# Kernel tuning notes

Measured on AMD Instinct MI355X. Metric: run time of the kernel, lower is better.

Reference implementation:

```python
import jax, jax.numpy as jnp
import numpy as np

VOCAB, DIM, HEADS, LAYERS = 32000, 1024, 16, 2
B, S = 2, 1024
HD = DIM // HEADS


def rmsnorm(x, g, eps=1e-6):
    return x * jax.lax.rsqrt(jnp.mean(x * x, axis=-1, keepdims=True) + eps) * g


def setup_inputs() -> dict:
    key = jax.random.key(0)
    ks = jax.random.split(key, 20)
    s = 0.02
    d = {
        "text_ids": jax.random.randint(ks[0], (B, S), 0, VOCAB),
        "embed": jax.random.normal(ks[1], (VOCAB, DIM), jnp.float32) * s,
        "g1": jnp.ones((LAYERS, DIM), jnp.float32),
        "wq": jax.random.normal(ks[2], (LAYERS, DIM, DIM), jnp.float32) * s,
        "bq": jnp.zeros((LAYERS, DIM), jnp.float32),
        "wk": jax.random.normal(ks[3], (LAYERS, DIM, DIM), jnp.float32) * s,
        "bk": jnp.zeros((LAYERS, DIM), jnp.float32),
        "wv": jax.random.normal(ks[4], (LAYERS, DIM, DIM), jnp.float32) * s,
        "bv": jnp.zeros((LAYERS, DIM), jnp.float32),
        "wo": jax.random.normal(ks[5], (LAYERS, DIM, DIM), jnp.float32) * s,
        "bo": jnp.zeros((LAYERS, DIM), jnp.float32),
        "g2": jnp.ones((LAYERS, DIM), jnp.float32),
        "w1": jax.random.normal(ks[6], (LAYERS, DIM, 4 * DIM), jnp.float32) * s,
        "b1": jnp.zeros((LAYERS, 4 * DIM), jnp.float32),
        "w2": jax.random.normal(ks[7], (LAYERS, 4 * DIM, DIM), jnp.float32) * s,
        "b2": jnp.zeros((LAYERS, DIM), jnp.float32),
        "gf": jnp.ones((DIM,), jnp.float32),
        "head_w": jax.random.normal(ks[8], (DIM, VOCAB), jnp.float32) * s,
        "head_b": jnp.zeros((VOCAB,), jnp.float32),
    }
    return d


def reference(text_ids, embed, g1, wq, bq, wk, bk, wv, bv, wo, bo,
              g2, w1, b1, w2, b2, gf, head_w, head_b):
    b, s = text_ids.shape
    x = embed[text_ids]                                   # [B,S,D]
    causal = jnp.tril(jnp.ones((s, s), dtype=bool))        # [S,S]
    scale = 1.0 / jnp.sqrt(jnp.asarray(HD, x.dtype))
    for l in range(LAYERS):
        # attention sublayer: x = x + attn(norm1(x))
        h = rmsnorm(x, g1[l])
        q = (h @ wq[l] + bq[l]).reshape(b, s, HEADS, HD)
        k = (h @ wk[l] + bk[l]).reshape(b, s, HEADS, HD)
        v = (h @ wv[l] + bv[l]).reshape(b, s, HEADS, HD)
        scores = jnp.einsum("bqhd,bkhd->bhqk", q, k) * scale
        scores = jnp.where(causal, scores, jnp.asarray(-1e30, scores.dtype))
        a = jax.nn.softmax(scores, axis=-1)
        o = jnp.einsum("bhqk,bkhd->bqhd", a, v).reshape(b, s, DIM)
        x = x + (o @ wo[l] + bo[l])
        # FFN sublayer: x = x + ffn(norm2(x)), SiLU MLP (MoE unused in source forward)
        h2 = rmsnorm(x, g2[l])
        x = x + (jax.nn.silu(h2 @ w1[l] + b1[l]) @ w2[l] + b2[l])
    x = rmsnorm(x, gf)
    return x.astype(jnp.float32) @ head_w + head_b         # [B,S,VOCAB]
```

## Files before the change

### kernel.cpp

```cpp
#include <hip/hip_runtime.h>

#define LAYERS 2
#define DIM 1024
#define HEADS 16
#define HD 64
#define BATCH 2
#define SEQ 1024
#define ROWS (BATCH * SEQ)
#define FFN (4 * DIM)
#define VOCAB 32000
#define QKVN (3 * DIM)

typedef unsigned short u16;
typedef short vshort8 __attribute__((ext_vector_type(8)));
typedef float f32x4 __attribute__((ext_vector_type(4)));

#define VMCNT(n) asm volatile("s_waitcnt vmcnt(" #n ")" ::: "memory")

__device__ __forceinline__ u16 f2bf(float f) {
  union { float f; unsigned u; } x{f};
  unsigned r = (x.u + 0x7fffu + ((x.u >> 16) & 1u)) >> 16;
  return (u16)r;
}

__device__ __forceinline__ void gll16(const void* g, u16* l) {
  __builtin_amdgcn_global_load_lds(
      (const __attribute__((address_space(1))) void*)g,
      (__attribute__((address_space(3))) void*)l, 16, 0, 0);
}

__device__ __forceinline__ int xcd_swizzle(int orig, int nwg) {
  int q = nwg >> 3, r = nwg & 7;
  int xcd = orig & 7;
  int base = (xcd < r) ? xcd * (q + 1) : r * (q + 1) + (xcd - r) * q;
  return base + (orig >> 3);
}

__device__ __forceinline__ void trans64(const float* __restrict__ src,
                                        u16* __restrict__ dst, int C, int R,
                                        int r0, int c0, int tid,
                                        u16 (*tl)[72]) {
  int lr = tid >> 4, lc4 = (tid & 15) * 4;
#pragma unroll
  for (int i = 0; i < 4; i++) {
    int row = lr + i * 16;
    float4 v = *(const float4*)&src[(size_t)(r0 + row) * C + c0 + lc4];
    ushort4 o{f2bf(v.x), f2bf(v.y), f2bf(v.z), f2bf(v.w)};
    *(ushort4*)&tl[row][lc4] = o;
  }
  __syncthreads();
#pragma unroll
  for (int i = 0; i < 2; i++) {
    int idx = tid + i * 256;
    int ci = idx >> 3, ri0 = (idx & 7) * 8;
    vshort8 o;
#pragma unroll
    for (int j = 0; j < 8; j++) o[j] = (short)tl[ri0 + j][ci];
    *(vshort8*)&dst[(size_t)(c0 + ci) * R + r0 + ri0] = o;
  }
}

__global__ __launch_bounds__(256) void transpose_all_kernel(
    const float* __restrict__ wq, const float* __restrict__ wk,
    const float* __restrict__ wv, const float* __restrict__ wo,
    const float* __restrict__ w1, const float* __restrict__ w2,
    const float* __restrict__ head_w, const float* __restrict__ bq,
    const float* __restrict__ bk, const float* __restrict__ bv,
    u16* __restrict__ wqkvT, u16* __restrict__ woT, u16* __restrict__ w1T,
    u16* __restrict__ w2T, u16* __restrict__ headT,
    float* __restrict__ bqkv) {
  __shared__ u16 tl[64][72];
  int bid = blockIdx.x, tid = threadIdx.x;
  if (bid >= 14144) {
    int t = (bid - 14144) * 256 + tid;
    int l = t / QKVN, c = t % QKVN;
    float v;
    if (c < DIM) v = bq[l * DIM + c];
    else if (c < 2 * DIM) v = bk[l * DIM + c - DIM];
    else v = bv[l * DIM + c - 2 * DIM];
    bqkv[(size_t)l * QKVN + c] = v;
    return;
  }
  const float* src;
  u16* dst;
  int R, C, r0, c0;
  if (bid < 2048) {
    int job = bid >> 8, tile = bid & 255;
    int l = job >> 2, wsel = job & 3;
    src = (wsel == 0 ? wq : wsel == 1 ? wk : wsel == 2 ? wv : wo) +
          (size_t)l * DIM * DIM;
    dst = (wsel < 3)
              ? wqkvT + (size_t)l * QKVN * DIM + (size_t)wsel * DIM * DIM
              : woT + (size_t)l * DIM * DIM;
    R = DIM; C = DIM;
    c0 = (tile & 15) * 64; r0 = (tile >> 4) * 64;
  } else if (bid < 4096) {
    int idx = bid - 2048;
    int l = idx >> 10, t = idx & 1023;
    src = w1 + (size_t)l * DIM * FFN;
    dst = w1T + (size_t)l * DIM * FFN;
    R = DIM; C = FFN;
    c0 = (t & 63) * 64; r0 = (t >> 6) * 64;
  } else if (bid < 6144) {
    int idx = bid - 4096;
    int l = idx >> 10, t = idx & 1023;
    src = w2 + (size_t)l * FFN * DIM;
    dst = w2T + (size_t)l * FFN * DIM;
    R = FFN; C = DIM;
    c0 = (t & 15) * 64; r0 = (t >> 4) * 64;
  } else {
    int t = bid - 6144;
    src = head_w; dst = headT;
    R = DIM; C = VOCAB;
    c0 = (t % 500) * 64; r0 = (t / 500) * 64;
  }
  trans64(src, dst, C, R, r0, c0, tid, tl);
}

__global__ __launch_bounds__(256) void embed_norm_kernel(
    const int* __restrict__ ids, const float* __restrict__ emb,
    const float* __restrict__ g, float* __restrict__ x, u16* __restrict__ h) {
  int row = blockIdx.x;
  int t = threadIdx.x;
  int id = ids[row];
  float4 v = ((const float4*)(emb + (size_t)id * DIM))[t];
  ((float4*)(x + (size_t)row * DIM))[t] = v;
  float ss = v.x * v.x + v.y * v.y + v.z * v.z + v.w * v.w;
  for (int off = 32; off > 0; off >>= 1) ss += __shfl_down(ss, off);
  __shared__ float part[4];
  if ((t & 63) == 0) part[t >> 6] = ss;
  __syncthreads();
  float tot = part[0] + part[1] + part[2] + part[3];
  float r = rsqrtf(tot / (float)DIM + 1e-6f);
  float4 gv = ((const float4*)g)[t];
  ushort4 o;
  o.x = f2bf(v.x * r * gv.x);
  o.y = f2bf(v.y * r * gv.y);
  o.z = f2bf(v.z * r * gv.z);
  o.w = f2bf(v.w * r * gv.w);
  *(ushort4*)(h + (size_t)row * DIM + t * 4) = o;
}

__global__ __launch_bounds__(256) void addnorm_kernel(
    float* __restrict__ x, const float* __restrict__ P0,
    const float* __restrict__ P1, const float* __restrict__ bias,
    const float* __restrict__ g, u16* __restrict__ h) {
  int row = blockIdx.x;
  int t = threadIdx.x;
  float4 v = ((const float4*)(x + (size_t)row * DIM))[t];
  float4 a = ((const float4*)(P0 + (size_t)row * DIM))[t];
  float4 b = ((const float4*)(P1 + (size_t)row * DIM))[t];
  float4 c = ((const float4*)bias)[t];
  v.x += a.x + b.x + c.x;
  v.y += a.y + b.y + c.y;
  v.z += a.z + b.z + c.z;
  v.w += a.w + b.w + c.w;
  ((float4*)(x + (size_t)row * DIM))[t] = v;
  float ss = v.x * v.x + v.y * v.y + v.z * v.z + v.w * v.w;
  for (int off = 32; off > 0; off >>= 1) ss += __shfl_down(ss, off);
  __shared__ float part[4];
  if ((t & 63) == 0) part[t >> 6] = ss;
  __syncthreads();
  float tot = part[0] + part[1] + part[2] + part[3];
  float r = rsqrtf(tot / (float)DIM + 1e-6f);
  float4 gv = ((const float4*)g)[t];
  ushort4 o;
  o.x = f2bf(v.x * r * gv.x);
  o.y = f2bf(v.y * r * gv.y);
  o.z = f2bf(v.z * r * gv.z);
  o.w = f2bf(v.w * r * gv.w);
  *(ushort4*)(h + (size_t)row * DIM + t * 4) = o;
}

template <int NMT, int OUTF32, int SILU, int VT>
__global__ __launch_bounds__(512, 2) void gemm256x128p_kernel(
    const u16* __restrict__ A, const u16* __restrict__ Wt,
    const float* __restrict__ bias, void* __restrict__ outv,
    u16* __restrict__ vt2, int M, int N, int K) {
  __shared__ u16 As[3][256 * 64];
  __shared__ u16 Bs[3][128 * 64];
  int nm = M >> 8, nn = N >> 7;
  int nwg = (NMT == 1) ? nm * nn : nn;
  int wg = xcd_swizzle(blockIdx.x, nwg);
  int mi0, ni;
  if (NMT == 1) { mi0 = wg % nm; ni = wg / nm; }
  else          { mi0 = 0; ni = wg; }
  int n0 = ni << 7;
  int tid = threadIdx.x, w = tid >> 6, lane = tid & 63;
  int wr = w >> 1, wc = w & 1;
  int r16 = lane & 15, g4 = lane >> 4;
  int srow8 = lane >> 3, sslot = lane & 7;
  const int NG = NMT * 16;

  f32x4 acc[4][4] = {};

  auto stage = [&](int g) {
    int buf = g % 3;
    int kt = g & 15;
    int mb = (mi0 + (g >> 4)) << 8;
#pragma unroll
    for (int j = 0; j < 4; j++) {
      int chunk = j * 8 + w;
      int row = chunk * 8 + srow8;
      int slot = sslot ^ (row & 7);
      gll16(A + (size_t)(mb + row) * K + kt * 64 + slot * 8,
            &As[buf][chunk * 512 + lane * 8]);
    }
#pragma unroll
    for (int j = 0; j < 2; j++) {
      int chunk = j * 8 + w;
      int row = chunk * 8 + srow8;
      int slot = sslot ^ (row & 7);
      gll16(Wt + (size_t)(n0 + row) * K + kt * 64 + slot * 8,
            &Bs[buf][chunk * 512 + lane * 8]);
    }
  };
  auto readA = [&](int buf, int mf, int kk) -> vshort8 {
    int row = wr * 64 + mf * 16 + r16;
    int slot = (kk * 4 + g4) ^ (row & 7);
    return *(const vshort8*)&As[buf][row * 64 + slot * 8];
  };
  auto readB = [&](int buf, int nf, int kk) -> vshort8 {
    int row = wc * 64 + nf * 16 + r16;
    int slot = (kk * 4 + g4) ^ (row & 7);
    return *(const vshort8*)&Bs[buf][row * 64 + slot * 8];
  };

  stage(0);
  stage(1);
  VMCNT(6);
  __builtin_amdgcn_s_barrier();

  vshort8 af[4][2], bf0[2][2], bf1[2][2];

  for (int mt = 0; mt < NMT; mt++) {
    for (int kt = 0; kt < 16; kt++) {
      int g = mt * 16 + kt;
      int buf = g % 3;
#pragma unroll
      for (int m = 0; m < 4; m++)
#pragma unroll
        for (int kk = 0; kk < 2; kk++) af[m][kk] = readA(buf, m, kk);
#pragma unroll
      for (int n = 0; n < 2; n++)
#pragma unroll
        for (int kk = 0; kk < 2; kk++) bf0[n][kk] = readB(buf, n, kk);
      bool staged = (g + 2 < NG);
      if (staged) stage(g + 2);
      __builtin_amdgcn_s_barrier();
      __builtin_amdgcn_s_setprio(1);
#pragma unroll
      for (int m = 0; m < 4; m++)
#pragma unroll
        for (int n = 0; n < 2; n++)
#pragma unroll
          for (int kk = 0; kk < 2; kk++)
            acc[m][n] = __builtin_amdgcn_mfma_f32_16x16x32_bf16(
                af[m][kk], bf0[n][kk], acc[m][n], 0, 0, 0);
      __builtin_amdgcn_s_setprio(0);
      __builtin_amdgcn_s_barrier();
#pragma unroll
      for (int n = 0; n < 2; n++)
#pragma unroll
        for (int kk = 0; kk < 2; kk++) bf1[n][kk] = readB(buf, 2 + n, kk);
      __builtin_amdgcn_s_barrier();
      __builtin_amdgcn_s_setprio(1);
#pragma unroll
      for (int m = 0; m < 4; m++)
#pragma unroll
        for (int n = 0; n < 2; n++)
#pragma unroll
          for (int kk = 0; kk < 2; kk++)
            acc[m][n + 2] = __builtin_amdgcn_mfma_f32_16x16x32_bf16(
                af[m][kk], bf1[n][kk], acc[m][n + 2], 0, 0, 0);
      __builtin_amdgcn_s_setprio(0);
      if (staged) { VMCNT(6); } else { VMCNT(0); }
      __builtin_amdgcn_s_barrier();
    }
    int m0e = (mi0 + mt) << 8;
#pragma unroll
    for (int m = 0; m < 4; m++) {
      int rowb = m0e + wr * 64 + m * 16 + g4 * 4;
#pragma unroll
      for (int n = 0; n < 4; n++) {
        int col = n0 + wc * 64 + n * 16 + r16;
        float b = bias[col];
        if (OUTF32) {
#pragma unroll
          for (int j = 0; j < 4; j++)
            ((float*)outv)[(size_t)(rowb + j) * N + col] = acc[m][n][j] + b;
        } else {
          u16 ov[4];
#pragma unroll
          for (int j = 0; j < 4; j++) {
            float v = acc[m][n][j] + b;
            if (SILU) v = v / (1.f + __expf(-v));
            ov[j] = f2bf(v);
          }
          if (VT && col >= 2 * DIM) {
            int dv = col - 2 * DIM;
            int hh = dv >> 6, dd = dv & 63;
            int bb = rowb >> 10, s = rowb & 1023;
            ushort4 o4{ov[0], ov[1], ov[2], ov[3]};
            *(ushort4*)&vt2[((((size_t)(bb * 16 + hh) * (SEQ / 8) + (s >> 3)) *
                                  64 + dd) * 8) + (s & 7)] = o4;
          } else {
#pragma unroll
            for (int j = 0; j < 4; j++)
              ((u16*)outv)[(size_t)(rowb + j) * N + col] = ov[j];
          }
        }
        if (NMT > 1) acc[m][n] = f32x4{0.f, 0.f, 0.f, 0.f};
      }
    }
  }
}

template <int OUTBF, int SILU, int SPLITK, int MFAST>
__global__ __launch_bounds__(256, 2) void gemm128_kernel(
    const u16* __restrict__ A, const u16* __restrict__ Wt,
    const float* __restrict__ bias, void* __restrict__ outv,
    float* __restrict__ pout1, int M, int N, int K) {
  __shared__ u16 As[2][128 * 64];
  __shared__ u16 Bs[2][128 * 64];
  int nm = M >> 7, nn = N >> 7, nwg = nm * nn;
  int wg = xcd_swizzle(blockIdx.x, SPLITK ? nwg * 2 : nwg);
  int ks = 0;
  if (SPLITK) { ks = wg >= nwg; wg -= ks * nwg; }
  int mi, ni;
  if (MFAST) { mi = wg % nm; ni = wg / nm; }
  else       { ni = wg % nn; mi = wg / nn; }
  int m0 = mi << 7, n0 = ni << 7;
  int kb = SPLITK ? ks * (K >> 1) : 0;
  int NTt = (SPLITK ? (K >> 1) : K) >> 6;
  int tid = threadIdx.x, wave = tid >> 6, lane = tid & 63;
  int wr = wave >> 1, wc = wave & 1;
  int r16 = lane & 15, g4 = lane >> 4;
  int lrow = lane >> 3, lslot = lane & 7;

  f32x4 acc[4][4] = {};

  auto stage = [&](int buf, int kt) {
#pragma unroll
    for (int i = 0; i < 4; i++) {
      int s = wave * 4 + i;
      int row = s * 8 + lrow;
      int slot = lslot ^ (row & 7);
      gll16(A + (size_t)(m0 + row) * K + kb + kt * 64 + slot * 8,
            &As[buf][s * 512 + lane * 8]);
    }
#pragma unroll
    for (int i = 0; i < 4; i++) {
      int s = wave * 4 + i;
      int row = s * 8 + lrow;
      int slot = lslot ^ (row & 7);
      gll16(Wt + (size_t)(n0 + row) * K + kb + kt * 64 + slot * 8,
            &Bs[buf][s * 512 + lane * 8]);
    }
  };

  stage(0, 0);
  VMCNT(0);
  __builtin_amdgcn_s_barrier();

  for (int t = 0; t < NTt; t++) {
    int cur = t & 1;
    if (t + 1 < NTt) stage(cur ^ 1, t + 1);
#pragma unroll
    for (int kk = 0; kk < 2; kk++) {
      vshort8 af[4], bf[4];
#pragma unroll
      for (int m = 0; m < 4; m++) {
        int r = wr * 64 + m * 16 + r16;
        int slot = (kk * 4 + g4) ^ (r & 7);
        af[m] = *(const vshort8*)&As[cur][r * 64 + slot * 8];
      }
#pragma unroll
      for (int n = 0; n < 4; n++) {
        int c = wc * 64 + n * 16 + r16;
        int slot = (kk * 4 + g4) ^ (c & 7);
        bf[n] = *(const vshort8*)&Bs[cur][c * 64 + slot * 8];
      }
#pragma unroll
      for (int m = 0; m < 4; m++)
#pragma unroll
        for (int n = 0; n < 4; n++)
          acc[m][n] = __builtin_amdgcn_mfma_f32_16x16x32_bf16(af[m], bf[n],
                                                              acc[m][n], 0, 0, 0);
    }
    VMCNT(0);
    __builtin_amdgcn_s_barrier();
  }

  if (SPLITK) {
    float* P = ks ? pout1 : (float*)outv;
#pragma unroll
    for (int m = 0; m < 4; m++) {
      int rowb = m0 + wr * 64 + m * 16 + g4 * 4;
#pragma unroll
      for (int n = 0; n < 4; n++) {
        int col = n0 + wc * 64 + n * 16 + r16;
#pragma unroll
        for (int j = 0; j < 4; j++)
          P[(size_t)(rowb + j) * N + col] = acc[m][n][j];
      }
    }
  } else {
#pragma unroll
    for (int m = 0; m < 4; m++) {
      int rowb = m0 + wr * 64 + m * 16 + g4 * 4;
#pragma unroll
      for (int n = 0; n < 4; n++) {
        int col = n0 + wc * 64 + n * 16 + r16;
        float b = bias[col];
#pragma unroll
        for (int j = 0; j < 4; j++) {
          float v = acc[m][n][j] + b;
          if (SILU) v = v / (1.f + __expf(-v));
          if (OUTBF)
            ((u16*)outv)[(size_t)(rowb + j) * N + col] = f2bf(v);
          else
            ((float*)outv)[(size_t)(rowb + j) * N + col] = v;
        }
      }
    }
  }
}

__global__ __launch_bounds__(512, 2) void gemm256p_kernel(
    const u16* __restrict__ A, const u16* __restrict__ Wt,
    const float* __restrict__ bias, float* __restrict__ out,
    int M, int N, int K) {
  __shared__ u16 As[2][256 * 64];
  __shared__ u16 Bs[2][256 * 64];
  int nn = N >> 8;
  int wg = xcd_swizzle(blockIdx.x, nn * 2);
  int mhalf = wg >= nn;
  int ni = mhalf ? wg - nn : wg;
  int n0 = ni << 8;
  int tid = threadIdx.x, w = tid >> 6, lane = tid & 63;
  int wr = w >> 2, wc = w & 3;
  int r16 = lane & 15, g4 = lane >> 4;
  int srow8 = lane >> 3, sslot = lane & 7;
  const int NTK = 16;
  const int NGT = 64;

  f32x4 acc[8][4] = {};

  auto stageA = [&](int buf, int mb, int kt, int hb, int j) {
    int chunk = j * 8 + w;
    int row = hb * 128 + chunk * 8 + srow8;
    int slot = sslot ^ (row & 7);
    gll16(A + (size_t)(mb + row) * K + kt * 64 + slot * 8,
          &As[buf][hb * 8192 + chunk * 512 + lane * 8]);
  };
  auto stageB = [&](int buf, int kt, int hb, int j) {
    int chunk = j * 8 + w;
    int row = hb * 128 + chunk * 8 + srow8;
    int slot = sslot ^ (row & 7);
    gll16(Wt + (size_t)(n0 + row) * K + kt * 64 + slot * 8,
          &Bs[buf][hb * 8192 + chunk * 512 + lane * 8]);
  };
  auto readA = [&](int buf, int mf, int kk) -> vshort8 {
    int row = mf * 32 + wr * 16 + r16;
    int slot = (kk * 4 + g4) ^ (row & 7);
    return *(const vshort8*)&As[buf][row * 64 + slot * 8];
  };
  auto readB = [&](int buf, int nf, int kk) -> vshort8 {
    int row = nf * 64 + wc * 16 + r16;
    int slot = (kk * 4 + g4) ^ (row & 7);
    return *(const vshort8*)&Bs[buf][row * 64 + slot * 8];
  };

  int mb0 = (mhalf * 4) << 8;
  stageA(0, mb0, 0, 0, 0); stageA(0, mb0, 0, 0, 1);
  stageB(0, 0, 0, 0);      stageB(0, 0, 0, 1);
  stageB(0, 0, 1, 0);      stageB(0, 0, 1, 1);
  stageA(0, mb0, 0, 1, 0); stageA(0, mb0, 0, 1, 1);
  VMCNT(4);
  __builtin_amdgcn_s_barrier();

  vshort8 af[4][2], bf0[2][2], bf1[2][2];

  for (int ti = 0; ti < 4; ti++) {
    int m0 = (mhalf * 4 + ti) << 8;
    for (int tt = 0; tt < NTK; tt++) {
      int gt = ti * NTK + tt;
      int cur = gt & 1, nxt = cur ^ 1;
      int gt1 = gt + 1;
      bool hn = gt1 < NGT;
      int kt1 = gt1 & (NTK - 1);
      int mb1 = (mhalf * 4 + (gt1 >> 4)) << 8;
#pragma unroll
      for (int m = 0; m < 4; m++)
#pragma unroll
        for (int kk = 0; kk < 2; kk++) af[m][kk] = readA(cur, m, kk);
#pragma unroll
      for (int n = 0; n < 2; n++)
#pragma unroll
        for (int kk = 0; kk < 2; kk++) bf0[n][kk] = readB(cur, n, kk);
      if (hn) {
        stageA(nxt, mb1, kt1, 0, 0); stageA(nxt, mb1, kt1, 0, 1);
        stageB(nxt, kt1, 0, 0);      stageB(nxt, kt1, 0, 1);
      }
      __builtin_amdgcn_s_barrier();
      __builtin_amdgcn_s_setprio(1);
#pragma unroll
      for (int m = 0; m < 4; m++)
#pragma unroll
        for (int n = 0; n < 2; n++)
#pragma unroll
          for (int kk = 0; kk < 2; kk++)
            acc[m][n] = __builtin_amdgcn_mfma_f32_16x16x32_bf16(
                af[m][kk], bf0[n][kk], acc[m][n], 0, 0, 0);
      __builtin_amdgcn_s_setprio(0);
      VMCNT(4);
      __builtin_amdgcn_s_barrier();
#pragma unroll
      for (int n = 0; n < 2; n++)
#pragma unroll
        for (int kk = 0; kk < 2; kk++) bf1[n][kk] = readB(cur, 2 + n, kk);
      __builtin_amdgcn_s_barrier();
      __builtin_amdgcn_s_setprio(1);
#pragma unroll
      for (int m = 0; m < 4; m++)
#pragma unroll
        for (int n = 0; n < 2; n++)
#pragma unroll
          for (int kk = 0; kk < 2; kk++)
            acc[m][n + 2] = __builtin_amdgcn_mfma_f32_16x16x32_bf16(
                af[m][kk], bf1[n][kk], acc[m][n + 2], 0, 0, 0);
      __builtin_amdgcn_s_setprio(0);
      __builtin_amdgcn_s_barrier();
#pragma unroll
      for (int m = 0; m < 4; m++)
#pragma unroll
        for (int kk = 0; kk < 2; kk++) af[m][kk] = readA(cur, 4 + m, kk);
      if (hn) {
        stageB(nxt, kt1, 1, 0);      stageB(nxt, kt1, 1, 1);
        stageA(nxt, mb1, kt1, 1, 0); stageA(nxt, mb1, kt1, 1, 1);
      }
      __builtin_amdgcn_s_barrier();
      __builtin_amdgcn_s_setprio(1);
#pragma unroll
      for (int m = 0; m < 4; m++)
#pragma unroll
        for (int n = 0; n < 2; n++)
#pragma unroll
          for (int kk = 0; kk < 2; kk++)
            acc[m + 4][n + 2] = __builtin_amdgcn_mfma_f32_16x16x32_bf16(
                af[m][kk], bf1[n][kk], acc[m + 4][n + 2], 0, 0, 0);
#pragma unroll
      for (int m = 0; m < 4; m++)
#pragma unroll
        for (int n = 0; n < 2; n++)
#pragma unroll
          for (int kk = 0; kk < 2; kk++)
            acc[m + 4][n] = __builtin_amdgcn_mfma_f32_16x16x32_bf16(
                af[m][kk], bf0[n][kk], acc[m + 4][n], 0, 0, 0);
      __builtin_amdgcn_s_setprio(0);
      VMCNT(4);
      __builtin_amdgcn_s_barrier();
    }
#pragma unroll
    for (int mf = 0; mf < 8; mf++) {
      int rowb = m0 + mf * 32 + wr * 16 + g4 * 4;
#pragma unroll
      for (int nf = 0; nf < 4; nf++) {
        int col = n0 + nf * 64 + wc * 16 + r16;
        float b = bias[col];
#pragma unroll
        for (int j = 0; j < 4; j++)
          out[(size_t)(rowb + j) * N + col] = acc[mf][nf][j] + b;
      }
    }
#pragma unroll
    for (int mf = 0; mf < 8; mf++)
#pragma unroll
      for (int nf = 0; nf < 4; nf++) acc[mf][nf] = f32x4{0.f, 0.f, 0.f, 0.f};
  }
}

__global__ __launch_bounds__(256) void attn_kernel(const u16* __restrict__ qkv,
                                                   const u16* __restrict__ vt2,
                                                   u16* __restrict__ o) {
  __shared__ u16 Ks[2][32 * 64];
  __shared__ u16 pl[4][16 * 40];
  int qblk = blockIdx.x, bh = blockIdx.y;
  int b = bh >> 4, h = bh & 15;
  int tid = threadIdx.x, w = tid >> 6, lane = tid & 63;
  int r16 = lane & 15, g4 = lane >> 4;
  int q0 = qblk * 64 + w * 16;

  const u16* qrow = qkv + ((size_t)(b * SEQ) + q0 + r16) * QKVN + h * HD;
  vshort8 aq0 = *(const vshort8*)(qrow + g4 * 8);
  vshort8 aq1 = *(const vshort8*)(qrow + 32 + g4 * 8);

  float mrun[4], lrun[4];
  f32x4 accO[4];
#pragma unroll
  for (int j = 0; j < 4; j++) { mrun[j] = -1e30f; lrun[j] = 0.f; }
#pragma unroll
  for (int d = 0; d < 4; d++) accO[d] = f32x4{0.f, 0.f, 0.f, 0.f};

  int nkvT = qblk * 2 + 2;
  auto stageK = [&](int buf, int kt) {
    int row = tid >> 3;
    int slot = (tid & 7) ^ (row & 7);
    gll16(qkv + ((size_t)(b * SEQ) + kt * 32 + row) * QKVN + DIM + h * HD + slot * 8,
          &Ks[buf][w * 512 + lane * 8]);
  };
  stageK(0, 0);
  __syncthreads();
  int buf = 0;
  for (int kt = 0; kt < nkvT; kt++) {
    int kv0 = kt * 32;
    if (kt + 1 < nkvT) stageK(buf ^ 1, kt + 1);
    if (kv0 <= q0 + 15) {
      int row0 = r16, row1 = 16 + r16;
      vshort8 bk00 = *(const vshort8*)&Ks[buf][row0 * 64 + ((0 + g4) ^ (row0 & 7)) * 8];
      vshort8 bk01 = *(const vshort8*)&Ks[buf][row0 * 64 + ((4 + g4) ^ (row0 & 7)) * 8];
      vshort8 bk10 = *(const vshort8*)&Ks[buf][row1 * 64 + ((0 + g4) ^ (row1 & 7)) * 8];
      vshort8 bk11 = *(const vshort8*)&Ks[buf][row1 * 64 + ((4 + g4) ^ (row1 & 7)) * 8];
      f32x4 s0 = {}, s1 = {};
      s0 = __builtin_amdgcn_mfma_f32_16x16x32_bf16(aq0, bk00, s0, 0, 0, 0);
      s0 = __builtin_amdgcn_mfma_f32_16x16x32_bf16(aq1, bk01, s0, 0, 0, 0);
      s1 = __builtin_amdgcn_mfma_f32_16x16x32_bf16(aq0, bk10, s1, 0, 0, 0);
      s1 = __builtin_amdgcn_mfma_f32_16x16x32_bf16(aq1, bk11, s1, 0, 0, 0);

#pragma unroll
      for (int j = 0; j < 4; j++) {
        int qg = q0 + g4 * 4 + j;
        float x0 = s0[j] * 0.125f;
        float x1 = s1[j] * 0.125f;
        if (kv0 + r16 > qg) x0 = -1e30f;
        if (kv0 + 16 + r16 > qg) x1 = -1e30f;
        float mx = fmaxf(x0, x1);
#pragma unroll
        for (int mm = 1; mm < 16; mm <<= 1) mx = fmaxf(mx, __shfl_xor(mx, mm));
        float mnew = fmaxf(mrun[j], mx);
        float alpha = __expf(mrun[j] - mnew);
        float p0 = __expf(x0 - mnew);
        float p1 = __expf(x1 - mnew);
        float rs = p0 + p1;
#pragma unroll
        for (int mm = 1; mm < 16; mm <<= 1) rs += __shfl_xor(rs, mm);
        lrun[j] = lrun[j] * alpha + rs;
        mrun[j] = mnew;
#pragma unroll
        for (int d = 0; d < 4; d++) accO[d][j] *= alpha;
        pl[w][(g4 * 4 + j) * 40 + r16] = f2bf(p0);
        pl[w][(g4 * 4 + j) * 40 + 16 + r16] = f2bf(p1);
      }
      asm volatile("s_waitcnt lgkmcnt(0)" ::: "memory");
      vshort8 ap = *(const vshort8*)&pl[w][r16 * 40 + g4 * 8];
      const u16* vbase = vt2 + (((size_t)bh * (SEQ / 8) + (kv0 >> 3) + g4) * 64) * 8;
#pragma unroll
      for (int d = 0; d < 4; d++) {
        vshort8 bv = *(const vshort8*)(vbase + (size_t)(d * 16 + r16) * 8);
        accO[d] = __builtin_amdgcn_mfma_f32_16x16x32_bf16(ap, bv, accO[d], 0, 0, 0);
      }
    }
    __syncthreads();
    buf ^= 1;
  }

#pragma unroll
  for (int j = 0; j < 4; j++) {
    float inv = 1.f / lrun[j];
    int row = q0 + g4 * 4 + j;
#pragma unroll
    for (int d = 0; d < 4; d++)
      o[((size_t)(b * SEQ) + row) * DIM + h * HD + d * 16 + r16] =
          f2bf(accO[d][j] * inv);
  }
}

extern "C" void kernel_launch(void* const* d_in, const int* in_sizes, int n_in,
                              void* d_out, int out_size, void* d_ws,
                              size_t ws_size, hipStream_t stream) {
  const int* ids = (const int*)d_in[0];
  const float* emb = (const float*)d_in[1];
  const float* g1 = (const float*)d_in[2];
  const float* wq = (const float*)d_in[3];
  const float* bq = (const float*)d_in[4];
  const float* wk = (const float*)d_in[5];
  const float* bk = (const float*)d_in[6];
  const float* wv = (const float*)d_in[7];
  const float* bv = (const float*)d_in[8];
  const float* wo = (const float*)d_in[9];
  const float* bo = (const float*)d_in[10];
  const float* g2 = (const float*)d_in[11];
  const float* w1 = (const float*)d_in[12];
  const float* b1 = (const float*)d_in[13];
  const float* w2 = (const float*)d_in[14];
  const float* b2 = (const float*)d_in[15];
  const float* gf = (const float*)d_in[16];
  const float* head_w = (const float*)d_in[17];
  const float* head_b = (const float*)d_in[18];
  float* out = (float*)d_out;

  char* ws = (char*)d_ws;
  size_t off = 0;
  auto alloc = [&](size_t bytes) -> char* {
    char* p = ws + off;
    off += (bytes + 255) & ~(size_t)255;
    return p;
  };
  u16* wqkvT = (u16*)alloc((size_t)LAYERS * QKVN * DIM * 2);
  u16* woT = (u16*)alloc((size_t)LAYERS * DIM * DIM * 2);
  u16* w1T = (u16*)alloc((size_t)LAYERS * DIM * FFN * 2);
  u16* w2T = (u16*)alloc((size_t)LAYERS * DIM * FFN * 2);
  u16* headT = (u16*)alloc((size_t)VOCAB * DIM * 2);
  float* bqkv = (float*)alloc((size_t)LAYERS * QKVN * 4);
  float* x = (float*)alloc((size_t)ROWS * DIM * 4);
  u16* h = (u16*)alloc((size_t)ROWS * DIM * 2);
  u16* qkvb = (u16*)alloc((size_t)ROWS * QKVN * 2);
  u16* vtb = (u16*)alloc((size_t)ROWS * DIM * 2);
  u16* ob = (u16*)alloc((size_t)ROWS * DIM * 2);
  u16* tb = (u16*)alloc((size_t)ROWS * FFN * 2);
  float* P0 = (float*)alloc((size_t)ROWS * DIM * 4);
  float* P1 = (float*)alloc((size_t)ROWS * DIM * 4);
  if (off > ws_size) return;

  transpose_all_kernel<<<14144 + 24, 256, 0, stream>>>(
      wq, wk, wv, wo, w1, w2, head_w, bq, bk, bv, wqkvT, woT, w1T, w2T, headT,
      bqkv);
  embed_norm_kernel<<<ROWS, 256, 0, stream>>>(ids, emb, g1, x, h);

  for (int l = 0; l < LAYERS; l++) {
    gemm256x128p_kernel<1, 0, 0, 1>
        <<<(ROWS / 256) * (QKVN / 128), 512, 0, stream>>>(
            h, wqkvT + (size_t)l * QKVN * DIM, bqkv + (size_t)l * QKVN,
            qkvb, vtb, ROWS, QKVN, DIM);
    attn_kernel<<<dim3(SEQ / 64, BATCH * HEADS), 256, 0, stream>>>(qkvb, vtb, ob);
    gemm128_kernel<0, 0, 1, 0>
        <<<2 * (ROWS / 128) * (DIM / 128), 256, 0, stream>>>(
            ob, woT + (size_t)l * DIM * DIM, nullptr, P0, P1, ROWS, DIM, DIM);
    addnorm_kernel<<<ROWS, 256, 0, stream>>>(
        x, P0, P1, bo + (size_t)l * DIM, g2 + (size_t)l * DIM, h);
    gemm256x128p_kernel<1, 0, 1, 0>
        <<<(ROWS / 256) * (FFN / 128), 512, 0, stream>>>(
            h, w1T + (size_t)l * DIM * FFN, b1 + (size_t)l * FFN, tb, nullptr,
            ROWS, FFN, DIM);
    gemm128_kernel<0, 0, 1, 0>
        <<<2 * (ROWS / 128) * (DIM / 128), 256, 0, stream>>>(
            tb, w2T + (size_t)l * DIM * FFN, nullptr, P0, P1, ROWS, DIM, FFN);
    addnorm_kernel<<<ROWS, 256, 0, stream>>>(
        x, P0, P1, b2 + (size_t)l * DIM,
        (l == LAYERS - 1) ? gf : (g1 + (size_t)(l + 1) * DIM), h);
  }
  gemm256p_kernel<<<(VOCAB / 256) * 2, 512, 0, stream>>>(
      h, headT, head_b, out, ROWS, VOCAB, DIM);
}
```

Measured before the change: 591.4 us.

## Use 4-way split-K for Wo/W2 GEMMs and fold embedding into prologue kernel

```diff
diff --git a/kernel.cpp b/kernel.cpp
--- a/kernel.cpp
+++ b/kernel.cpp
@@ -60,25 +60,48 @@
   }
 }
 
-__global__ __launch_bounds__(256) void transpose_all_kernel(
+__global__ __launch_bounds__(256) void prologue_kernel(
     const float* __restrict__ wq, const float* __restrict__ wk,
     const float* __restrict__ wv, const float* __restrict__ wo,
     const float* __restrict__ w1, const float* __restrict__ w2,
     const float* __restrict__ head_w, const float* __restrict__ bq,
     const float* __restrict__ bk, const float* __restrict__ bv,
-    u16* __restrict__ wqkvT, u16* __restrict__ woT, u16* __restrict__ w1T,
-    u16* __restrict__ w2T, u16* __restrict__ headT,
-    float* __restrict__ bqkv) {
+    const int* __restrict__ ids, const float* __restrict__ emb,
+    const float* __restrict__ g1, u16* __restrict__ wqkvT,
+    u16* __restrict__ woT, u16* __restrict__ w1T, u16* __restrict__ w2T,
+    u16* __restrict__ headT, float* __restrict__ bqkv, float* __restrict__ x,
+    u16* __restrict__ h) {
   __shared__ u16 tl[64][72];
+  __shared__ float part[4];
   int bid = blockIdx.x, tid = threadIdx.x;
-  if (bid >= 14144) {
-    int t = (bid - 14144) * 256 + tid;
+  if (bid >= 6144 && bid < 6168) {
+    int t = (bid - 6144) * 256 + tid;
     int l = t / QKVN, c = t % QKVN;
     float v;
     if (c < DIM) v = bq[l * DIM + c];
     else if (c < 2 * DIM) v = bk[l * DIM + c - DIM];
     else v = bv[l * DIM + c - 2 * DIM];
     bqkv[(size_t)l * QKVN + c] = v;
+    return;
+  }
+  if (bid >= 6168 && bid < 8216) {
+    int row = bid - 6168;
+    int id = ids[row];
+    float4 v = ((const float4*)(emb + (size_t)id * DIM))[tid];
+    ((float4*)(x + (size_t)row * DIM))[tid] = v;
+    float ss = v.x * v.x + v.y * v.y + v.z * v.z + v.w * v.w;
+    for (int off = 32; off > 0; off >>= 1) ss += __shfl_down(ss, off);
+    if ((tid & 63) == 0) part[tid >> 6] = ss;
+    __syncthreads();
+    float tot = part[0] + part[1] + part[2] + part[3];
+    float r = rsqrtf(tot / (float)DIM + 1e-6f);
+    float4 gv = ((const float4*)g1)[tid];
+    ushort4 o;
+    o.x = f2bf(v.x * r * gv.x);
+    o.y = f2bf(v.y * r * gv.y);
+    o.z = f2bf(v.z * r * gv.z);
+    o.w = f2bf(v.w * r * gv.w);
+    *(ushort4*)(h + (size_t)row * DIM + tid * 4) = o;
     return;
   }
   const float* src;
@@ -109,7 +132,7 @@
     R = FFN; C = DIM;
     c0 = (t & 15) * 64; r0 = (t >> 4) * 64;
   } else {
-    int t = bid - 6144;
+    int t = bid - 8216;
     src = head_w; dst = headT;
     R = DIM; C = VOCAB;
     c0 = (t % 500) * 64; r0 = (t / 500) * 64;
@@ -117,44 +140,21 @@
   trans64(src, dst, C, R, r0, c0, tid, tl);
 }
 
-__global__ __launch_bounds__(256) void embed_norm_kernel(
-    const int* __restrict__ ids, const float* __restrict__ emb,
-    const float* __restrict__ g, float* __restrict__ x, u16* __restrict__ h) {
-  int row = blockIdx.x;
-  int t = threadIdx.x;
-  int id = ids[row];
-  float4 v = ((const float4*)(emb + (size_t)id * DIM))[t];
-  ((float4*)(x + (size_t)row * DIM))[t] = v;
-  float ss = v.x * v.x + v.y * v.y + v.z * v.z + v.w * v.w;
-  for (int off = 32; off > 0; off >>= 1) ss += __shfl_down(ss, off);
-  __shared__ float part[4];
-  if ((t & 63) == 0) part[t >> 6] = ss;
-  __syncthreads();
-  float tot = part[0] + part[1] + part[2] + part[3];
-  float r = rsqrtf(tot / (float)DIM + 1e-6f);
-  float4 gv = ((const float4*)g)[t];
-  ushort4 o;
-  o.x = f2bf(v.x * r * gv.x);
-  o.y = f2bf(v.y * r * gv.y);
-  o.z = f2bf(v.z * r * gv.z);
-  o.w = f2bf(v.w * r * gv.w);
-  *(ushort4*)(h + (size_t)row * DIM + t * 4) = o;
-}
-
+template <int NP>
 __global__ __launch_bounds__(256) void addnorm_kernel(
-    float* __restrict__ x, const float* __restrict__ P0,
-    const float* __restrict__ P1, const float* __restrict__ bias,
-    const float* __restrict__ g, u16* __restrict__ h) {
+    float* __restrict__ x, const float* __restrict__ P,
+    const float* __restrict__ bias, const float* __restrict__ g,
+    u16* __restrict__ h) {
   int row = blockIdx.x;
   int t = threadIdx.x;
   float4 v = ((const float4*)(x + (size_t)row * DIM))[t];
-  float4 a = ((const float4*)(P0 + (size_t)row * DIM))[t];
-  float4 b = ((const float4*)(P1 + (size_t)row * DIM))[t];
   float4 c = ((const float4*)bias)[t];
-  v.x += a.x + b.x + c.x;
-  v.y += a.y + b.y + c.y;
-  v.z += a.z + b.z + c.z;
-  v.w += a.w + b.w + c.w;
+  v.x += c.x; v.y += c.y; v.z += c.z; v.w += c.w;
+#pragma unroll
+  for (int p = 0; p < NP; p++) {
+    float4 a = ((const float4*)(P + (size_t)p * ROWS * DIM + (size_t)row * DIM))[t];
+    v.x += a.x; v.y += a.y; v.z += a.z; v.w += a.w;
+  }
   ((float4*)(x + (size_t)row * DIM))[t] = v;
   float ss = v.x * v.x + v.y * v.y + v.z * v.z + v.w * v.w;
   for (int off = 32; off > 0; off >>= 1) ss += __shfl_down(ss, off);
@@ -316,23 +316,20 @@
   }
 }
 
-template <int OUTBF, int SILU, int SPLITK, int MFAST>
-__global__ __launch_bounds__(256, 2) void gemm128_kernel(
+template <int NS>
+__global__ __launch_bounds__(256, 2) void gemm128sk_kernel(
     const u16* __restrict__ A, const u16* __restrict__ Wt,
-    const float* __restrict__ bias, void* __restrict__ outv,
-    float* __restrict__ pout1, int M, int N, int K) {
+    float* __restrict__ P, int M, int N, int K) {
   __shared__ u16 As[2][128 * 64];
   __shared__ u16 Bs[2][128 * 64];
   int nm = M >> 7, nn = N >> 7, nwg = nm * nn;
-  int wg = xcd_swizzle(blockIdx.x, SPLITK ? nwg * 2 : nwg);
-  int ks = 0;
-  if (SPLITK) { ks = wg >= nwg; wg -= ks * nwg; }
-  int mi, ni;
-  if (MFAST) { mi = wg % nm; ni = wg / nm; }
-  else       { ni = wg % nn; mi = wg / nn; }
+  int wg = xcd_swizzle(blockIdx.x, nwg * NS);
+  int ks = wg / nwg;
+  wg -= ks * nwg;
+  int ni = wg % nn, mi = wg / nn;
   int m0 = mi << 7, n0 = ni << 7;
-  int kb = SPLITK ? ks * (K >> 1) : 0;
-  int NTt = (SPLITK ? (K >> 1) : K) >> 6;
+  int kb = ks * (K / NS);
+  int NTt = (K / NS) >> 6;
   int tid = threadIdx.x, wave = tid >> 6, lane = tid & 63;
   int wr = wave >> 1, wc = wave & 1;
   int r16 = lane & 15, g4 = lane >> 4;
@@ -392,37 +389,16 @@
     __builtin_amdgcn_s_barrier();
   }
 
-  if (SPLITK) {
-    float* P = ks ? pout1 : (float*)outv;
-#pragma unroll
-    for (int m = 0; m < 4; m++) {
-      int rowb = m0 + wr * 64 + m * 16 + g4 * 4;
-#pragma unroll
-      for (int n = 0; n < 4; n++) {
-        int col = n0 + wc * 64 + n * 16 + r16;
-#pragma unroll
-        for (int j = 0; j < 4; j++)
-          P[(size_t)(rowb + j) * N + col] = acc[m][n][j];
-      }
-    }
-  } else {
-#pragma unroll
-    for (int m = 0; m < 4; m++) {
-      int rowb = m0 + wr * 64 + m * 16 + g4 * 4;
-#pragma unroll
-      for (int n = 0; n < 4; n++) {
-        int col = n0 + wc * 64 + n * 16 + r16;
-        float b = bias[col];
-#pragma unroll
-        for (int j = 0; j < 4; j++) {
-          float v = acc[m][n][j] + b;
-          if (SILU) v = v / (1.f + __expf(-v));
-          if (OUTBF)
-            ((u16*)outv)[(size_t)(rowb + j) * N + col] = f2bf(v);
-          else
-            ((float*)outv)[(size_t)(rowb + j) * N + col] = v;
-        }
-      }
+  float* Pk = P + (size_t)ks * M * N;
+#pragma unroll
+  for (int m = 0; m < 4; m++) {
+    int rowb = m0 + wr * 64 + m * 16 + g4 * 4;
+#pragma unroll
+    for (int n = 0; n < 4; n++) {
+      int col = n0 + wc * 64 + n * 16 + r16;
+#pragma unroll
+      for (int j = 0; j < 4; j++)
+        Pk[(size_t)(rowb + j) * N + col] = acc[m][n][j];
     }
   }
 }
@@ -435,8 +411,7 @@
   __shared__ u16 Bs[2][256 * 64];
   int nn = N >> 8;
   int wg = xcd_swizzle(blockIdx.x, nn * 2);
-  int mhalf = wg >= nn;
-  int ni = mhalf ? wg - nn : wg;
+  int ni = wg >> 1, mhalf = wg & 1;
   int n0 = ni << 8;
   int tid = threadIdx.x, w = tid >> 6, lane = tid & 63;
   int wr = w >> 2, wc = w & 3;
@@ -719,14 +694,12 @@
   u16* vtb = (u16*)alloc((size_t)ROWS * DIM * 2);
   u16* ob = (u16*)alloc((size_t)ROWS * DIM * 2);
   u16* tb = (u16*)alloc((size_t)ROWS * FFN * 2);
-  float* P0 = (float*)alloc((size_t)ROWS * DIM * 4);
-  float* P1 = (float*)alloc((size_t)ROWS * DIM * 4);
+  float* P = (float*)alloc((size_t)4 * ROWS * DIM * 4);
   if (off > ws_size) return;
 
-  transpose_all_kernel<<<14144 + 24, 256, 0, stream>>>(
-      wq, wk, wv, wo, w1, w2, head_w, bq, bk, bv, wqkvT, woT, w1T, w2T, headT,
-      bqkv);
-  embed_norm_kernel<<<ROWS, 256, 0, stream>>>(ids, emb, g1, x, h);
+  prologue_kernel<<<16216, 256, 0, stream>>>(
+      wq, wk, wv, wo, w1, w2, head_w, bq, bk, bv, ids, emb, g1, wqkvT, woT,
+      w1T, w2T, headT, bqkv, x, h);
 
   for (int l = 0; l < LAYERS; l++) {
     gemm256x128p_kernel<1, 0, 0, 1>
@@ -734,20 +707,20 @@
             h, wqkvT + (size_t)l * QKVN * DIM, bqkv + (size_t)l * QKVN,
             qkvb, vtb, ROWS, QKVN, DIM);
     attn_kernel<<<dim3(SEQ / 64, BATCH * HEADS), 256, 0, stream>>>(qkvb, vtb, ob);
-    gemm128_kernel<0, 0, 1, 0>
-        <<<2 * (ROWS / 128) * (DIM / 128), 256, 0, stream>>>(
-            ob, woT + (size_t)l * DIM * DIM, nullptr, P0, P1, ROWS, DIM, DIM);
-    addnorm_kernel<<<ROWS, 256, 0, stream>>>(
-        x, P0, P1, bo + (size_t)l * DIM, g2 + (size_t)l * DIM, h);
+    gemm128sk_kernel<4>
+        <<<4 * (ROWS / 128) * (DIM / 128), 256, 0, stream>>>(
+            ob, woT + (size_t)l * DIM * DIM, P, ROWS, DIM, DIM);
+    addnorm_kernel<4><<<ROWS, 256, 0, stream>>>(
+        x, P, bo + (size_t)l * DIM, g2 + (size_t)l * DIM, h);
     gemm256x128p_kernel<1, 0, 1, 0>
         <<<(ROWS / 256) * (FFN / 128), 512, 0, stream>>>(
             h, w1T + (size_t)l * DIM * FFN, b1 + (size_t)l * FFN, tb, nullptr,
             ROWS, FFN, DIM);
-    gemm128_kernel<0, 0, 1, 0>
-        <<<2 * (ROWS / 128) * (DIM / 128), 256, 0, stream>>>(
-            tb, w2T + (size_t)l * DIM * FFN, nullptr, P0, P1, ROWS, DIM, FFN);
-    addnorm_kernel<<<ROWS, 256, 0, stream>>>(
-        x, P0, P1, b2 + (size_t)l * DIM,
+    gemm128sk_kernel<4>
+        <<<4 * (ROWS / 128) * (DIM / 128), 256, 0, stream>>>(
+            tb, w2T + (size_t)l * DIM * FFN, P, ROWS, DIM, FFN);
+    addnorm_kernel<4><<<ROWS, 256, 0, stream>>>(
+        x, P, b2 + (size_t)l * DIM,
         (l == LAYERS - 1) ? gf : (g1 + (size_t)(l + 1) * DIM), h);
   }
   gemm256p_kernel<<<(VOCAB / 256) * 2, 512, 0, stream>>>(
```

New measurement: 558.6 us, median of 2. 5.6% less time.
